# Kernel optimization log

Measured on AMD Instinct MI355X. Metric: run time of the kernel, lower is better.

The kernel has to match this reference:

```python
import jax, jax.numpy as jnp
import numpy as np

N = 8192      # nodes
F = 256       # in_features
H = 64        # hidden_dim
NEG = -9e15   # mask fill value from the torch source
EPS = 1e-5    # LayerNorm eps (torch default)


def setup_inputs() -> dict:
    key = jax.random.key(0)
    ks = jax.random.split(key, 6)
    x = jax.random.normal(ks[0], (N, F), jnp.float32)
    adj = jax.random.randint(ks[1], (N, N), 0, 2, jnp.int32)
    # Linear params (xavier-ish scale, zero bias as in reset_parameters)
    Wt = jax.random.normal(ks[2], (H, F), jnp.float32) * (1.0 / np.sqrt(F))
    bt = jnp.zeros((H,), jnp.float32)
    Wa = jax.random.normal(ks[3], (1, H), jnp.float32) * (1.0 / np.sqrt(H))
    ba = jnp.zeros((1,), jnp.float32)
    Wp = jax.random.normal(ks[4], (F, H), jnp.float32) * (1.0 / np.sqrt(H))
    bp = jnp.zeros((F,), jnp.float32)
    gamma = jnp.ones((F,), jnp.float32)
    beta = jnp.zeros((F,), jnp.float32)
    return dict(x=x, adj=adj, Wt=Wt, bt=bt, Wa=Wa, ba=ba,
                Wp=Wp, bp=bp, gamma=gamma, beta=beta)


def reference(x, adj, Wt, bt, Wa, ba, Wp, bp, gamma, beta):
    # h = feature_transform(x): [N, H]
    h = x @ Wt.T + bt
    # per-source-node scalar score, expanded over all N columns: [N, 1]
    s = jax.nn.leaky_relu(h @ Wa.T + ba, negative_slope=0.2)
    # adjacency-masked softmax over neighbors (dim=1); s broadcasts to [N, N]
    scores = jnp.where(adj > 0, s, jnp.float32(NEG))
    w = jax.nn.softmax(scores, axis=1)            # [N, N]
    # dropout inactive at inference -> identity
    neighbor = w @ h                               # [N, H]
    tf = neighbor @ Wp.T + bp                      # [N, F]
    # residual + LayerNorm
    y = x + tf
    mu = jnp.mean(y, axis=-1, keepdims=True)
    var = jnp.var(y, axis=-1, keepdims=True)
    return gamma * (y - mu) * jax.lax.rsqrt(var + EPS) + beta
```

## Files before the change

### kernel.cpp

```cpp
#include <hip/hip_runtime.h>
#include <stdint.h>

#define NN 8192
#define FF 256
#define HH 64

typedef __attribute__((ext_vector_type(8))) short bf16x8;
typedef __attribute__((ext_vector_type(4))) float f32x4;

__device__ __forceinline__ uint16_t f2bf(float f) {
  union { float f; uint32_t i; } c; c.f = f;
  uint32_t r = c.i + 0x7FFFu + ((c.i >> 16) & 1u);
  return (uint16_t)(r >> 16);
}

__global__ __launch_bounds__(256) void k1_h(
    const float* __restrict__ x, const float* __restrict__ Wt,
    const float* __restrict__ bt, float* __restrict__ h,
    float* __restrict__ nb_sum, int* __restrict__ deg_g) {
  __shared__ float wtT[256 * 65];
  __shared__ float sbt[64];
  const int t = threadIdx.x;
  const int lane = t & 63;
  const int w = t >> 6;

  for (int i = 0; i < 64; ++i)
    wtT[t * 65 + i] = Wt[(size_t)i * FF + t];
  if (t < 64) sbt[t] = bt[t];
  __syncthreads();

  const int r0 = blockIdx.x * 32 + w * 8;
  const float binit = sbt[lane];
  float acc[8];
#pragma unroll
  for (int r = 0; r < 8; ++r) acc[r] = binit;

  for (int f4 = 0; f4 < FF; f4 += 4) {
    float4 xs[8];
#pragma unroll
    for (int r = 0; r < 8; ++r)
      xs[r] = *(const float4*)(x + (size_t)(r0 + r) * FF + f4);
    const float wt0 = wtT[(f4 + 0) * 65 + lane];
    const float wt1 = wtT[(f4 + 1) * 65 + lane];
    const float wt2 = wtT[(f4 + 2) * 65 + lane];
    const float wt3 = wtT[(f4 + 3) * 65 + lane];
#pragma unroll
    for (int r = 0; r < 8; ++r)
      acc[r] += xs[r].x * wt0 + xs[r].y * wt1 + xs[r].z * wt2 + xs[r].w * wt3;
  }
#pragma unroll
  for (int r = 0; r < 8; ++r)
    h[(size_t)(r0 + r) * HH + lane] = acc[r];

  float4 z = {0.f, 0.f, 0.f, 0.f};
  float4* nbz = (float4*)(nb_sum + (size_t)blockIdx.x * 32 * HH);
  for (int i = t; i < 512; i += 256) nbz[i] = z;
  if (t < 32) deg_g[blockIdx.x * 32 + t] = 0;
}

__global__ __launch_bounds__(256) void k1b_hT(
    const float* __restrict__ h, uint16_t* __restrict__ hT) {
  __shared__ float s[64][65];
  const int t = threadIdx.x;
  const int n0 = blockIdx.x * 64;
  for (int i = 0; i < 16; ++i) {
    int idx = i * 256 + t;
    int r = idx >> 6, c = idx & 63;
    s[r][c] = h[(size_t)(n0 + r) * HH + c];
  }
  __syncthreads();
  for (int i = 0; i < 16; ++i) {
    int idx = i * 256 + t;
    int c = idx >> 6, n = idx & 63;
    hT[(size_t)c * NN + n0 + n] = f2bf(s[n][c]);
  }
}

__global__ __launch_bounds__(256) void k2_attn(
    const int* __restrict__ adj, const uint16_t* __restrict__ hT,
    float* __restrict__ nb_sum, int* __restrict__ deg_g) {
  __shared__ float s_part[4][16][64];
  __shared__ int   s_deg[16];

  const int t    = threadIdx.x;
  const int w    = t >> 6;
  const int lane = t & 63;
  const int m    = lane & 15;
  const int q    = lane >> 4;
  const int g    = blockIdx.x >> 1;
  const int half = blockIdx.x & 1;
  const int row0 = g * 16;

  if (t < 16) s_deg[t] = 0;
  __syncthreads();

  const int kbeg = half * (NN / 2) + w * (NN / 8);
  const int kend = kbeg + (NN / 8);

  f32x4 acc0 = 0, acc1 = 0, acc2 = 0, acc3 = 0;
  int degm = 0;
  const int* __restrict__ arow = adj + (size_t)(row0 + m) * NN;
  const uint16_t* __restrict__ hrow = hT + (size_t)m * NN;

  for (int kb = kbeg; kb < kend; kb += 64) {
    const int k0 = kb + q * 8;
    const int k1 = k0 + 32;
    int4 a0 = *(const int4*)(arow + k0);
    int4 a1 = *(const int4*)(arow + k0 + 4);
    int4 a2 = *(const int4*)(arow + k1);
    int4 a3 = *(const int4*)(arow + k1 + 4);
    bf16x8 b0 = *(const bf16x8*)(hrow + k0);
    bf16x8 b1 = *(const bf16x8*)(hrow + 16 * NN + k0);
    bf16x8 b2 = *(const bf16x8*)(hrow + 32 * NN + k0);
    bf16x8 b3 = *(const bf16x8*)(hrow + 48 * NN + k0);
    bf16x8 c0 = *(const bf16x8*)(hrow + k1);
    bf16x8 c1 = *(const bf16x8*)(hrow + 16 * NN + k1);
    bf16x8 c2 = *(const bf16x8*)(hrow + 32 * NN + k1);
    bf16x8 c3 = *(const bf16x8*)(hrow + 48 * NN + k1);
    bf16x8 afA;
    afA[0] = a0.x ? (short)0x3F80 : (short)0;
    afA[1] = a0.y ? (short)0x3F80 : (short)0;
    afA[2] = a0.z ? (short)0x3F80 : (short)0;
    afA[3] = a0.w ? (short)0x3F80 : (short)0;
    afA[4] = a1.x ? (short)0x3F80 : (short)0;
    afA[5] = a1.y ? (short)0x3F80 : (short)0;
    afA[6] = a1.z ? (short)0x3F80 : (short)0;
    afA[7] = a1.w ? (short)0x3F80 : (short)0;
    bf16x8 afB;
    afB[0] = a2.x ? (short)0x3F80 : (short)0;
    afB[1] = a2.y ? (short)0x3F80 : (short)0;
    afB[2] = a2.z ? (short)0x3F80 : (short)0;
    afB[3] = a2.w ? (short)0x3F80 : (short)0;
    afB[4] = a3.x ? (short)0x3F80 : (short)0;
    afB[5] = a3.y ? (short)0x3F80 : (short)0;
    afB[6] = a3.z ? (short)0x3F80 : (short)0;
    afB[7] = a3.w ? (short)0x3F80 : (short)0;
    acc0 = __builtin_amdgcn_mfma_f32_16x16x32_bf16(afA, b0, acc0, 0, 0, 0);
    acc1 = __builtin_amdgcn_mfma_f32_16x16x32_bf16(afA, b1, acc1, 0, 0, 0);
    acc2 = __builtin_amdgcn_mfma_f32_16x16x32_bf16(afA, b2, acc2, 0, 0, 0);
    acc3 = __builtin_amdgcn_mfma_f32_16x16x32_bf16(afA, b3, acc3, 0, 0, 0);
    acc0 = __builtin_amdgcn_mfma_f32_16x16x32_bf16(afB, c0, acc0, 0, 0, 0);
    acc1 = __builtin_amdgcn_mfma_f32_16x16x32_bf16(afB, c1, acc1, 0, 0, 0);
    acc2 = __builtin_amdgcn_mfma_f32_16x16x32_bf16(afB, c2, acc2, 0, 0, 0);
    acc3 = __builtin_amdgcn_mfma_f32_16x16x32_bf16(afB, c3, acc3, 0, 0, 0);
    degm += a0.x + a0.y + a0.z + a0.w + a1.x + a1.y + a1.z + a1.w;
    degm += a2.x + a2.y + a2.z + a2.w + a3.x + a3.y + a3.z + a3.w;
  }

  degm += __shfl_down(degm, 32, 64);
  degm += __shfl_down(degm, 16, 64);
  if (lane < 16) atomicAdd(&s_deg[lane], degm);

#pragma unroll
  for (int rg = 0; rg < 4; ++rg) {
    s_part[w][q * 4 + rg][ 0 + m] = acc0[rg];
    s_part[w][q * 4 + rg][16 + m] = acc1[rg];
    s_part[w][q * 4 + rg][32 + m] = acc2[rg];
    s_part[w][q * 4 + rg][48 + m] = acc3[rg];
  }
  __syncthreads();

  for (int idx = t; idx < 16 * 64; idx += 256) {
    int r = idx >> 6, c = idx & 63;
    float s = s_part[0][r][c] + s_part[1][r][c] +
              s_part[2][r][c] + s_part[3][r][c];
    atomicAdd(&nb_sum[(size_t)(row0 + r) * HH + c], s);
  }
  if (t < 16) atomicAdd(&deg_g[row0 + t], s_deg[t]);
}

__global__ __launch_bounds__(256) void k3_epi(
    const float* __restrict__ x, const float* __restrict__ nb_sum,
    const int* __restrict__ deg_g, const float* __restrict__ Wp,
    const float* __restrict__ bp, const float* __restrict__ gamma,
    const float* __restrict__ beta, float* __restrict__ out) {
  __shared__ float s_nb[16][64];
  __shared__ float s_y[16 * 256];

  const int t    = threadIdx.x;
  const int w    = t >> 6;
  const int lane = t & 63;
  const int row0 = blockIdx.x * 16;

  for (int idx = t; idx < 16 * 64; idx += 256) {
    int r = idx >> 6, c = idx & 63;
    int d = deg_g[row0 + r];
    float s = nb_sum[(size_t)(row0 + r) * HH + c];
    s_nb[r][c] = (d > 0) ? s / (float)d : 0.f;
  }
  __syncthreads();

  {
    const int f = t;
    float wp[64];
    const float* wrow = Wp + (size_t)f * HH;
#pragma unroll
    for (int j = 0; j < 16; ++j) {
      float4 v = *(const float4*)(wrow + j * 4);
      wp[j * 4 + 0] = v.x; wp[j * 4 + 1] = v.y;
      wp[j * 4 + 2] = v.z; wp[j * 4 + 3] = v.w;
    }
    const float bpf = bp[f];
    for (int r = 0; r < 16; ++r) {
      float a = bpf;
#pragma unroll
      for (int k = 0; k < 64; k += 4) {
        float4 nv = *(const float4*)&s_nb[r][k];
        a += nv.x * wp[k] + nv.y * wp[k + 1] + nv.z * wp[k + 2] + nv.w * wp[k + 3];
      }
      float y = x[(size_t)(row0 + r) * FF + f] + a;
      s_y[r * 256 + f] = y;
    }
  }
  __syncthreads();

  for (int i = 0; i < 4; ++i) {
    const int r = w * 4 + i;
    float4 v = *(const float4*)&s_y[r * 256 + lane * 4];
    float sum = v.x + v.y + v.z + v.w;
    float ss  = v.x * v.x + v.y * v.y + v.z * v.z + v.w * v.w;
#pragma unroll
    for (int o = 32; o >= 1; o >>= 1) {
      sum += __shfl_xor(sum, o, 64);
      ss  += __shfl_xor(ss, o, 64);
    }
    const float mu  = sum * (1.0f / 256.0f);
    const float var = ss * (1.0f / 256.0f) - mu * mu;
    const float rs  = rsqrtf(var + 1e-5f);
    const int f0 = lane * 4;
    float4 g = *(const float4*)(gamma + f0);
    float4 b = *(const float4*)(beta + f0);
    float4 o4;
    o4.x = g.x * (v.x - mu) * rs + b.x;
    o4.y = g.y * (v.y - mu) * rs + b.y;
    o4.z = g.z * (v.z - mu) * rs + b.z;
    o4.w = g.w * (v.w - mu) * rs + b.w;
    *(float4*)(out + (size_t)(row0 + r) * FF + f0) = o4;
  }
}

extern "C" void kernel_launch(void* const* d_in, const int* in_sizes, int n_in,
                              void* d_out, int out_size, void* d_ws, size_t ws_size,
                              hipStream_t stream) {
  const float* x     = (const float*)d_in[0];
  const int*   adj   = (const int*)d_in[1];
  const float* Wt    = (const float*)d_in[2];
  const float* bt    = (const float*)d_in[3];
  const float* Wp    = (const float*)d_in[6];
  const float* bp    = (const float*)d_in[7];
  const float* gamma = (const float*)d_in[8];
  const float* beta  = (const float*)d_in[9];
  float* out = (float*)d_out;

  uint16_t* hT     = (uint16_t*)d_ws;
  float*    nb_sum = (float*)((char*)d_ws + (1u << 20));
  int*      deg_g  = (int*)((char*)d_ws + (3u << 20));
  float*    h      = (float*)((char*)d_ws + (3u << 20) + (1u << 18));

  k1_h  <<<256, 256, 0, stream>>>(x, Wt, bt, h, nb_sum, deg_g);
  k1b_hT<<<128, 256, 0, stream>>>(h, hT);
  k2_attn<<<1024, 256, 0, stream>>>(adj, hT, nb_sum, deg_g);
  k3_epi<<<512, 256, 0, stream>>>(x, nb_sum, deg_g, Wp, bp, gamma, beta, out);
}
```

Measured before the change: 443.4 us.

## Fuse transpose into h kernel, replace atomics with per-half partials, pack adjacency conversion

Folds the separate bf16 transpose kernel into the h projection kernel: h is transposed through shared memory and written directly as bf16 hT, which removes one launch and an fp32 h round trip. The attention kernel now writes each half's partial sums and degrees to separate buffers instead of doing atomic adds, so the zero-initialisation step goes away and the epilogue adds the two halves. The adjacency-to-bf16 mask conversion packs int pairs and multiplies by the bf16 one pattern, which cuts per-element selects and also yields the degree count. The packed trick assumes adjacency values are 0 or 1.

```diff
diff --git a/kernel.cpp b/kernel.cpp
--- a/kernel.cpp
+++ b/kernel.cpp
@@ -16,10 +16,10 @@
 
 __global__ __launch_bounds__(256) void k1_h(
     const float* __restrict__ x, const float* __restrict__ Wt,
-    const float* __restrict__ bt, float* __restrict__ h,
-    float* __restrict__ nb_sum, int* __restrict__ deg_g) {
+    const float* __restrict__ bt, uint16_t* __restrict__ hT) {
   __shared__ float wtT[256 * 65];
   __shared__ float sbt[64];
+  __shared__ uint16_t s_tr[64][34];
   const int t = threadIdx.x;
   const int lane = t & 63;
   const int w = t >> 6;
@@ -29,7 +29,8 @@
   if (t < 64) sbt[t] = bt[t];
   __syncthreads();
 
-  const int r0 = blockIdx.x * 32 + w * 8;
+  const int n0 = blockIdx.x * 32;
+  const int r0 = n0 + w * 8;
   const float binit = sbt[lane];
   float acc[8];
 #pragma unroll
@@ -48,37 +49,24 @@
     for (int r = 0; r < 8; ++r)
       acc[r] += xs[r].x * wt0 + xs[r].y * wt1 + xs[r].z * wt2 + xs[r].w * wt3;
   }
+
 #pragma unroll
   for (int r = 0; r < 8; ++r)
-    h[(size_t)(r0 + r) * HH + lane] = acc[r];
-
-  float4 z = {0.f, 0.f, 0.f, 0.f};
-  float4* nbz = (float4*)(nb_sum + (size_t)blockIdx.x * 32 * HH);
-  for (int i = t; i < 512; i += 256) nbz[i] = z;
-  if (t < 32) deg_g[blockIdx.x * 32 + t] = 0;
-}
-
-__global__ __launch_bounds__(256) void k1b_hT(
-    const float* __restrict__ h, uint16_t* __restrict__ hT) {
-  __shared__ float s[64][65];
-  const int t = threadIdx.x;
-  const int n0 = blockIdx.x * 64;
-  for (int i = 0; i < 16; ++i) {
+    s_tr[lane][w * 8 + r] = f2bf(acc[r]);
+  __syncthreads();
+#pragma unroll
+  for (int i = 0; i < 4; ++i) {
     int idx = i * 256 + t;
-    int r = idx >> 6, c = idx & 63;
-    s[r][c] = h[(size_t)(n0 + r) * HH + c];
-  }
-  __syncthreads();
-  for (int i = 0; i < 16; ++i) {
-    int idx = i * 256 + t;
-    int c = idx >> 6, n = idx & 63;
-    hT[(size_t)c * NN + n0 + n] = f2bf(s[n][c]);
+    int c = idx >> 4;
+    int d = idx & 15;
+    uint32_t v = (uint32_t)s_tr[c][2 * d] | ((uint32_t)s_tr[c][2 * d + 1] << 16);
+    *(uint32_t*)(hT + (size_t)c * NN + n0 + 2 * d) = v;
   }
 }
 
 __global__ __launch_bounds__(256) void k2_attn(
     const int* __restrict__ adj, const uint16_t* __restrict__ hT,
-    float* __restrict__ nb_sum, int* __restrict__ deg_g) {
+    float* __restrict__ nb_part, int* __restrict__ deg_part) {
   __shared__ float s_part[4][16][64];
   __shared__ int   s_deg[16];
 
@@ -98,7 +86,7 @@
   const int kend = kbeg + (NN / 8);
 
   f32x4 acc0 = 0, acc1 = 0, acc2 = 0, acc3 = 0;
-  int degm = 0;
+  uint32_t degp = 0;
   const int* __restrict__ arow = adj + (size_t)(row0 + m) * NN;
   const uint16_t* __restrict__ hrow = hT + (size_t)m * NN;
 
@@ -117,36 +105,35 @@
     bf16x8 c1 = *(const bf16x8*)(hrow + 16 * NN + k1);
     bf16x8 c2 = *(const bf16x8*)(hrow + 32 * NN + k1);
     bf16x8 c3 = *(const bf16x8*)(hrow + 48 * NN + k1);
-    bf16x8 afA;
-    afA[0] = a0.x ? (short)0x3F80 : (short)0;
-    afA[1] = a0.y ? (short)0x3F80 : (short)0;
-    afA[2] = a0.z ? (short)0x3F80 : (short)0;
-    afA[3] = a0.w ? (short)0x3F80 : (short)0;
-    afA[4] = a1.x ? (short)0x3F80 : (short)0;
-    afA[5] = a1.y ? (short)0x3F80 : (short)0;
-    afA[6] = a1.z ? (short)0x3F80 : (short)0;
-    afA[7] = a1.w ? (short)0x3F80 : (short)0;
-    bf16x8 afB;
-    afB[0] = a2.x ? (short)0x3F80 : (short)0;
-    afB[1] = a2.y ? (short)0x3F80 : (short)0;
-    afB[2] = a2.z ? (short)0x3F80 : (short)0;
-    afB[3] = a2.w ? (short)0x3F80 : (short)0;
-    afB[4] = a3.x ? (short)0x3F80 : (short)0;
-    afB[5] = a3.y ? (short)0x3F80 : (short)0;
-    afB[6] = a3.z ? (short)0x3F80 : (short)0;
-    afB[7] = a3.w ? (short)0x3F80 : (short)0;
-    acc0 = __builtin_amdgcn_mfma_f32_16x16x32_bf16(afA, b0, acc0, 0, 0, 0);
-    acc1 = __builtin_amdgcn_mfma_f32_16x16x32_bf16(afA, b1, acc1, 0, 0, 0);
-    acc2 = __builtin_amdgcn_mfma_f32_16x16x32_bf16(afA, b2, acc2, 0, 0, 0);
-    acc3 = __builtin_amdgcn_mfma_f32_16x16x32_bf16(afA, b3, acc3, 0, 0, 0);
-    acc0 = __builtin_amdgcn_mfma_f32_16x16x32_bf16(afB, c0, acc0, 0, 0, 0);
-    acc1 = __builtin_amdgcn_mfma_f32_16x16x32_bf16(afB, c1, acc1, 0, 0, 0);
-    acc2 = __builtin_amdgcn_mfma_f32_16x16x32_bf16(afB, c2, acc2, 0, 0, 0);
-    acc3 = __builtin_amdgcn_mfma_f32_16x16x32_bf16(afB, c3, acc3, 0, 0, 0);
-    degm += a0.x + a0.y + a0.z + a0.w + a1.x + a1.y + a1.z + a1.w;
-    degm += a2.x + a2.y + a2.z + a2.w + a3.x + a3.y + a3.z + a3.w;
-  }
-
+    uint32_t p0 = (uint32_t)a0.x | ((uint32_t)a0.y << 16);
+    uint32_t p1 = (uint32_t)a0.z | ((uint32_t)a0.w << 16);
+    uint32_t p2 = (uint32_t)a1.x | ((uint32_t)a1.y << 16);
+    uint32_t p3 = (uint32_t)a1.z | ((uint32_t)a1.w << 16);
+    uint32_t p4 = (uint32_t)a2.x | ((uint32_t)a2.y << 16);
+    uint32_t p5 = (uint32_t)a2.z | ((uint32_t)a2.w << 16);
+    uint32_t p6 = (uint32_t)a3.x | ((uint32_t)a3.y << 16);
+    uint32_t p7 = (uint32_t)a3.z | ((uint32_t)a3.w << 16);
+    union U { bf16x8 v; uint32_t u[4]; } afA, afB;
+    afA.u[0] = p0 * 0x3F80u;
+    afA.u[1] = p1 * 0x3F80u;
+    afA.u[2] = p2 * 0x3F80u;
+    afA.u[3] = p3 * 0x3F80u;
+    afB.u[0] = p4 * 0x3F80u;
+    afB.u[1] = p5 * 0x3F80u;
+    afB.u[2] = p6 * 0x3F80u;
+    afB.u[3] = p7 * 0x3F80u;
+    degp += p0 + p1 + p2 + p3 + p4 + p5 + p6 + p7;
+    acc0 = __builtin_amdgcn_mfma_f32_16x16x32_bf16(afA.v, b0, acc0, 0, 0, 0);
+    acc1 = __builtin_amdgcn_mfma_f32_16x16x32_bf16(afA.v, b1, acc1, 0, 0, 0);
+    acc2 = __builtin_amdgcn_mfma_f32_16x16x32_bf16(afA.v, b2, acc2, 0, 0, 0);
+    acc3 = __builtin_amdgcn_mfma_f32_16x16x32_bf16(afA.v, b3, acc3, 0, 0, 0);
+    acc0 = __builtin_amdgcn_mfma_f32_16x16x32_bf16(afB.v, c0, acc0, 0, 0, 0);
+    acc1 = __builtin_amdgcn_mfma_f32_16x16x32_bf16(afB.v, c1, acc1, 0, 0, 0);
+    acc2 = __builtin_amdgcn_mfma_f32_16x16x32_bf16(afB.v, c2, acc2, 0, 0, 0);
+    acc3 = __builtin_amdgcn_mfma_f32_16x16x32_bf16(afB.v, c3, acc3, 0, 0, 0);
+  }
+
+  int degm = (int)(degp & 0xFFFFu) + (int)(degp >> 16);
   degm += __shfl_down(degm, 32, 64);
   degm += __shfl_down(degm, 16, 64);
   if (lane < 16) atomicAdd(&s_deg[lane], degm);
@@ -160,18 +147,19 @@
   }
   __syncthreads();
 
+  float* __restrict__ dst = nb_part + ((size_t)half * NN + row0) * HH;
   for (int idx = t; idx < 16 * 64; idx += 256) {
     int r = idx >> 6, c = idx & 63;
     float s = s_part[0][r][c] + s_part[1][r][c] +
               s_part[2][r][c] + s_part[3][r][c];
-    atomicAdd(&nb_sum[(size_t)(row0 + r) * HH + c], s);
-  }
-  if (t < 16) atomicAdd(&deg_g[row0 + t], s_deg[t]);
+    dst[(size_t)r * HH + c] = s;
+  }
+  if (t < 16) deg_part[half * NN + row0 + t] = s_deg[t];
 }
 
 __global__ __launch_bounds__(256) void k3_epi(
-    const float* __restrict__ x, const float* __restrict__ nb_sum,
-    const int* __restrict__ deg_g, const float* __restrict__ Wp,
+    const float* __restrict__ x, const float* __restrict__ nb_part,
+    const int* __restrict__ deg_part, const float* __restrict__ Wp,
     const float* __restrict__ bp, const float* __restrict__ gamma,
     const float* __restrict__ beta, float* __restrict__ out) {
   __shared__ float s_nb[16][64];
@@ -184,8 +172,9 @@
 
   for (int idx = t; idx < 16 * 64; idx += 256) {
     int r = idx >> 6, c = idx & 63;
-    int d = deg_g[row0 + r];
-    float s = nb_sum[(size_t)(row0 + r) * HH + c];
+    int d = deg_part[row0 + r] + deg_part[NN + row0 + r];
+    float s = nb_part[(size_t)(row0 + r) * HH + c] +
+              nb_part[(size_t)(NN + row0 + r) * HH + c];
     s_nb[r][c] = (d > 0) ? s / (float)d : 0.f;
   }
   __syncthreads();
@@ -252,13 +241,11 @@
   const float* beta  = (const float*)d_in[9];
   float* out = (float*)d_out;
 
-  uint16_t* hT     = (uint16_t*)d_ws;
-  float*    nb_sum = (float*)((char*)d_ws + (1u << 20));
-  int*      deg_g  = (int*)((char*)d_ws + (3u << 20));
-  float*    h      = (float*)((char*)d_ws + (3u << 20) + (1u << 18));
-
-  k1_h  <<<256, 256, 0, stream>>>(x, Wt, bt, h, nb_sum, deg_g);
-  k1b_hT<<<128, 256, 0, stream>>>(h, hT);
-  k2_attn<<<1024, 256, 0, stream>>>(adj, hT, nb_sum, deg_g);
-  k3_epi<<<512, 256, 0, stream>>>(x, nb_sum, deg_g, Wp, bp, gamma, beta, out);
-}
+  uint16_t* hT       = (uint16_t*)d_ws;
+  float*    nb_part  = (float*)((char*)d_ws + (1u << 20));
+  int*      deg_part = (int*)((char*)d_ws + (5u << 20));
+
+  k1_h  <<<256,  256, 0, stream>>>(x, Wt, bt, hT);
+  k2_attn<<<1024, 256, 0, stream>>>(adj, hT, nb_part, deg_part);
+  k3_epi <<<512,  256, 0, stream>>>(x, nb_part, deg_part, Wp, bp, gamma, beta, out);
+}
```

After: 450.4 us. No clear change (+1.6%).
